# Kernel tuning notes

Measured on AMD Instinct MI355X. Metric: run time of the kernel, lower is better.

Reference implementation:

```python
import jax, jax.numpy as jnp
import numpy as np

N_CLASSES = 1000
FEAT_DIM = 256
N = 65536


def setup_inputs() -> dict:
    key = jax.random.key(0)
    k1, k2, k3 = jax.random.split(key, 3)
    gt = jax.random.randint(k1, (N, N_CLASSES), 0, 2, dtype=jnp.int32)
    features = jax.random.normal(k2, (N, FEAT_DIM), dtype=jnp.float32)
    centers = jax.random.normal(k3, (N_CLASSES, FEAT_DIM), dtype=jnp.float32)
    return {"gt": gt, "features": features, "centers": centers}


def reference(gt, features, centers):
    # loss = (1/N) * sum_c sum_{i : gt[i,c] > 0} ||features[i] - centers[c]||^2
    # Vectorized via ||f||^2 + ||c||^2 - 2 f.c  (replaces the per-class python loop)
    mask = (gt > 0).astype(features.dtype)                      # [N, C]
    f_sq = jnp.sum(features * features, axis=1)                 # [N]
    c_sq = jnp.sum(centers * centers, axis=1)                   # [C]
    cross = features @ centers.T                                # [N, C]
    dist = f_sq[:, None] + c_sq[None, :] - 2.0 * cross          # [N, C]
    num_instances = features.shape[0]
    return jnp.sum(mask * dist) / num_instances
```

## Files before the change

kernel.cpp:

```cpp
#include <hip/hip_runtime.h>
#include <stdint.h>

#define N_ROWS 65536
#define N_CLS  1000
#define KPAD   1024
#define FEAT   256
#define MT     64
#define NSTG   32
#define NIT    16

typedef short bf16x8 __attribute__((ext_vector_type(8)));
typedef float f32x4  __attribute__((ext_vector_type(4)));

__device__ __forceinline__ ushort f32_to_bf16_rne(float f) {
    union { float f; uint32_t u; } x; x.f = f;
    uint32_t u = x.u + 0x7FFFu + ((x.u >> 16) & 1u);
    return (ushort)(u >> 16);
}

__global__ __launch_bounds__(256) void prep_kernel(const float* __restrict__ centers,
                                                   ushort* __restrict__ Bfrag,
                                                   float* __restrict__ csq,
                                                   float* __restrict__ out) {
    const int c = blockIdx.x;
    const int n = threadIdx.x;
    float v = 0.f;
    if (c < N_CLS) v = centers[(size_t)c * FEAT + n];

    const int s    = c >> 5;
    const int quad = (c >> 3) & 3;
    const int j    = c & 7;
    const int w    = n >> 6;
    const int nt   = (n >> 4) & 3;
    const int ml   = n & 15;
    const int lane = quad * 16 + ml;
    const size_t idx = (((size_t)(s * 4 + w) * 4 + nt) * 64 + lane) * 8 + j;
    Bfrag[idx] = f32_to_bf16_rne(v);

    float sq = v * v;
    #pragma unroll
    for (int off = 32; off > 0; off >>= 1) sq += __shfl_down(sq, off);
    __shared__ float red[4];
    if ((threadIdx.x & 63) == 0) red[threadIdx.x >> 6] = sq;
    __syncthreads();
    if (threadIdx.x == 0) {
        csq[c] = red[0] + red[1] + red[2] + red[3];
        if (c == 0) out[0] = 0.f;
    }
}


__global__ __launch_bounds__(256) void compress_kernel(const int* __restrict__ gt,
                                                       const float* __restrict__ csq,
                                                       ushort* __restrict__ bitmask,
                                                       float* __restrict__ rowcnt,
                                                       float* __restrict__ t2row) {
    __shared__ float csqS[KPAD];
    const int tid  = threadIdx.x;
    *(float4*)&csqS[tid * 4] = *(const float4*)&csq[tid * 4];
    __syncthreads();
    const int lane = tid & 63;
    const int wid  = blockIdx.x * 4 + (tid >> 6);

    float4 cs[4];
    #pragma unroll
    for (int j = 0; j < 4; j++) cs[j] = *(const float4*)&csqS[j * 256 + lane * 4];
    const bool v3 = (768 + lane * 4) < N_CLS;

    auto ldrow = [&](int row, int4 (&d)[4]) {
        const int* g = gt + (size_t)row * N_CLS + lane * 4;
        d[0] = *(const int4*)(g);
        d[1] = *(const int4*)(g + 256);
        d[2] = *(const int4*)(g + 512);
        d[3] = v3 ? *(const int4*)(g + 768) : make_int4(0, 0, 0, 0);
    };
    auto proc = [&](int row, const int4 (&d)[4]) {
        uint32_t p =
              (uint32_t)d[0].x        | ((uint32_t)d[0].y << 1)  | ((uint32_t)d[0].z << 2)  | ((uint32_t)d[0].w << 3)
            | ((uint32_t)d[1].x << 4) | ((uint32_t)d[1].y << 5)  | ((uint32_t)d[1].z << 6)  | ((uint32_t)d[1].w << 7)
            | ((uint32_t)d[2].x << 8) | ((uint32_t)d[2].y << 9)  | ((uint32_t)d[2].z << 10) | ((uint32_t)d[2].w << 11)
            | ((uint32_t)d[3].x << 12)| ((uint32_t)d[3].y << 13) | ((uint32_t)d[3].z << 14) | ((uint32_t)d[3].w << 15);
        float t = (float)d[0].x * cs[0].x + (float)d[0].y * cs[0].y
                + (float)d[0].z * cs[0].z + (float)d[0].w * cs[0].w
                + (float)d[1].x * cs[1].x + (float)d[1].y * cs[1].y
                + (float)d[1].z * cs[1].z + (float)d[1].w * cs[1].w
                + (float)d[2].x * cs[2].x + (float)d[2].y * cs[2].y
                + (float)d[2].z * cs[2].z + (float)d[2].w * cs[2].w
                + (float)d[3].x * cs[3].x + (float)d[3].y * cs[3].y
                + (float)d[3].z * cs[3].z + (float)d[3].w * cs[3].w;
        int rc = __popc(p);
        #pragma unroll
        for (int off = 1; off < 64; off <<= 1) {
            rc += __shfl_xor(rc, off);
            t  += __shfl_xor(t, off);
        }
        bitmask[(size_t)row * 64 + lane] = (ushort)p;
        if (lane == 0) { rowcnt[row] = (float)rc; t2row[row] = t; }
    };

    int4 dP[4], dQ[4];
    ldrow(wid, dP);
    ldrow(wid + 8192, dQ);
    #pragma unroll
    for (int rr = 0; rr < 8; rr += 2) {
        if (rr + 2 < 8) { proc(wid + rr * 8192, dP); ldrow(wid + (rr + 2) * 8192, dP); }
        else              proc(wid + rr * 8192, dP);
        if (rr + 3 < 8) { proc(wid + (rr + 1) * 8192, dQ); ldrow(wid + (rr + 3) * 8192, dQ); }
        else              proc(wid + (rr + 1) * 8192, dQ);
    }
}

__global__ __launch_bounds__(256, 3) void main2_kernel(const ushort* __restrict__ bitmask,
                                                       const float* __restrict__ features,
                                                       const ushort* __restrict__ Bfrag,
                                                       const float* __restrict__ rowcnt,
                                                       const float* __restrict__ t2row,
                                                       float* __restrict__ out) {
    __shared__ uint32_t bmS[MT * 33];
    __shared__ float    rcS[MT], t2S[MT], blockred[4];

    const int tid  = threadIdx.x;
    const int lane = tid & 63;
    const int w    = tid >> 6;
    const int ml   = lane & 15;
    const int quad = lane >> 4;
    const int m0   = blockIdx.x * MT;

    const uint32_t* bm = (const uint32_t*)bitmask + (size_t)m0 * 32;
    #pragma unroll
    for (int i = 0; i < 8; i++) {
        int idx = i * 256 + tid;
        bmS[(idx >> 5) * 33 + (idx & 31)] = bm[idx];
    }
    if (tid < MT) rcS[tid] = rowcnt[m0 + tid];
    else if (tid < 2 * MT) t2S[tid - MT] = t2row[m0 + tid - MT];
    __syncthreads();

    f32x4 acc[4][4];
    #pragma unroll
    for (int i = 0; i < 4; i++)
        #pragma unroll
        for (int j = 0; j < 4; j++)
            #pragma unroll
            for (int k = 0; k < 4; k++) acc[i][j][k] = 0.f;

    const ushort* bb = Bfrag + ((size_t)w * 4 * 64 + lane) * 8;
    auto ld_B = [&](int s, bf16x8 (&b)[4]) {
        const ushort* p = bb + (size_t)s * 8192;
        b[0] = *(const bf16x8*)(p);
        b[1] = *(const bf16x8*)(p + 512);
        b[2] = *(const bf16x8*)(p + 1024);
        b[3] = *(const bf16x8*)(p + 1536);
    };

    auto dostage = [&](int s, const bf16x8 (&b)[4]) {
        const int dw = (s & 7) * 4 + quad;
        const int sb = (s >> 3) * 4;
        #pragma unroll
        for (int mt = 0; mt < 4; mt++) {
            const uint32_t W = bmS[(mt * 16 + ml) * 33 + dw];
            union { uint32_t u[4]; bf16x8 v; } a;
            #pragma unroll
            for (int p = 0; p < 4; p++) {
                const int b0 = (p < 2) ? (sb + 2 * p) : (16 + sb + 2 * (p - 2));
                a.u[p] = ((W >> b0) & 1u) * 0x3F80u
                       | ((W >> (b0 + 1)) & 1u) * 0x3F800000u;
            }
            #pragma unroll
            for (int nt = 0; nt < 4; nt++)
                acc[mt][nt] = __builtin_amdgcn_mfma_f32_16x16x32_bf16(
                    a.v, b[nt], acc[mt][nt], 0, 0, 0);
        }
    };

    bf16x8 BfP[4], BfQ[4];
    ld_B(0, BfP);
    ld_B(1, BfQ);
    for (int s = 0; s < NSTG; s += 2) {
        dostage(s, BfP);
        if (s + 2 < NSTG) ld_B(s + 2, BfP);
        dostage(s + 1, BfQ);
        if (s + 3 < NSTG) ld_B(s + 3, BfQ);
    }

    float part = 0.f;
    #pragma unroll
    for (int mt = 0; mt < 4; mt++) {
        #pragma unroll
        for (int nt = 0; nt < 4; nt++) {
            const int n = w * 64 + nt * 16 + ml;
            #pragma unroll
            for (int reg = 0; reg < 4; reg++) {
                const int ri = mt * 16 + quad * 4 + reg;
                const float f = features[(size_t)(m0 + ri) * FEAT + n];
                part += f * (rcS[ri] * f - 2.f * acc[mt][nt][reg]) + t2S[ri] * (1.f / 256.f);
            }
        }
    }
    #pragma unroll
    for (int off = 32; off > 0; off >>= 1) part += __shfl_down(part, off);
    if (lane == 0) blockred[w] = part;
    __syncthreads();
    if (tid == 0)
        atomicAdd(out, (blockred[0] + blockred[1] + blockred[2] + blockred[3]) *
                           (1.f / (float)N_ROWS));
}

__global__ __launch_bounds__(256, 3) void fused_kernel(const int* __restrict__ gt,
                                                       const float* __restrict__ features,
                                                       const ushort* __restrict__ Bfrag,
                                                       const float* __restrict__ csq,
                                                       float* __restrict__ out) {
    __shared__ ushort As[2 * 2 * 4 * 64 * 8];
    __shared__ float  csqS[KPAD];
    __shared__ float  rcS[256], t2S[256], rowcnt[MT], t2row[MT], blockred[4];

    const int tid  = threadIdx.x;
    const int m0   = blockIdx.x * MT;
    const int r    = tid >> 2;
    const int kc   = tid & 3;
    const int lane = tid & 63;
    const int w    = tid >> 6;
    const int ml   = lane & 15;
    const int quad = lane >> 4;

    f32x4 acc[4][4];
    #pragma unroll
    for (int i = 0; i < 4; i++)
        #pragma unroll
        for (int j = 0; j < 4; j++)
            #pragma unroll
            for (int k = 0; k < 4; k++) acc[i][j][k] = 0.f;

    int   rci = 0;
    float t2  = 0.f;
    const int* gtrow = gt + (size_t)(m0 + r) * N_CLS;

    const int mt_w = r >> 4, ml_w = r & 15;
    const int ks_w = kc >> 1, qb = (kc & 1) * 2;
    const int xw   = (ml_w >> 3) | (ks_w << 1) | ((kc & 1) << 2);
    const int slot0 = (((ks_w * 4 + mt_w) * 64) + (qb * 16 + ml_w)) ^ xw;
    const int slot1 = (((ks_w * 4 + mt_w) * 64) + ((qb + 1) * 16 + ml_w)) ^ xw;
    ushort* const wptr0 = As + slot0 * 8;
    ushort* const wptr1 = As + slot1 * 8;

    const int xr0 = ((lane >> 3) & 1) | (((lane >> 5) & 1) << 2);
    const int lx0 = (lane ^ xr0) * 8;
    const int lx1 = (lane ^ (xr0 | 2)) * 8;

    auto load_gt = [&](int it, int (&vv)[16]) {
        const int kb = it * 64 + kc * 16;
        if (kb + 16 <= N_CLS) {
            const int4* p = (const int4*)(gtrow + kb);
            int4 a0 = p[0], a1 = p[1], a2 = p[2], a3 = p[3];
            vv[0]=a0.x;  vv[1]=a0.y;  vv[2]=a0.z;  vv[3]=a0.w;
            vv[4]=a1.x;  vv[5]=a1.y;  vv[6]=a1.z;  vv[7]=a1.w;
            vv[8]=a2.x;  vv[9]=a2.y;  vv[10]=a2.z; vv[11]=a2.w;
            vv[12]=a3.x; vv[13]=a3.y; vv[14]=a3.z; vv[15]=a3.w;
        } else {
            #pragma unroll
            for (int j = 0; j < 16; j++) {
                int k = kb + j;
                vv[j] = (k < N_CLS) ? gtrow[k] : 0;
            }
        }
    };

    auto convert_store = [&](int buf, int it, const int (&vv)[16]) {
        const int kb = it * 64 + kc * 16;
        const float4* cp = (const float4*)&csqS[kb];
        float4 q0 = cp[0], q1 = cp[1], q2 = cp[2], q3 = cp[3];
        float cs[16] = {q0.x,q0.y,q0.z,q0.w, q1.x,q1.y,q1.z,q1.w,
                        q2.x,q2.y,q2.z,q2.w, q3.x,q3.y,q3.z,q3.w};
        uint32_t u[8];
        #pragma unroll
        for (int j = 0; j < 8; j++)
            u[j] = (uint32_t)(vv[2*j] + (vv[2*j+1] << 16)) * 0x3F80u;
        #pragma unroll
        for (int j = 0; j < 16; j++) { rci += vv[j]; t2 += (float)vv[j] * cs[j]; }
        uint4* d0 = (uint4*)(wptr0 + buf * 4096);
        uint4* d1 = (uint4*)(wptr1 + buf * 4096);
        *d0 = make_uint4(u[0], u[1], u[2], u[3]);
        *d1 = make_uint4(u[4], u[5], u[6], u[7]);
    };

    const ushort* bbase = Bfrag + ((size_t)w * 4) * 64 * 8 + (size_t)lane * 8;
    auto mfma_iter = [&](int buf, int it) {
        bf16x8 b0[4], b1[4];
        const ushort* p0 = bbase + (size_t)(it * 2 + 0) * (4 * 4 * 64 * 8);
        const ushort* p1 = bbase + (size_t)(it * 2 + 1) * (4 * 4 * 64 * 8);
        #pragma unroll
        for (int nt = 0; nt < 4; ++nt) b0[nt] = *(const bf16x8*)(p0 + nt * 64 * 8);
        #pragma unroll
        for (int nt = 0; nt < 4; ++nt) b1[nt] = *(const bf16x8*)(p1 + nt * 64 * 8);
        #pragma unroll
        for (int ks = 0; ks < 2; ++ks) {
            const int lx = ks ? lx1 : lx0;
            bf16x8 af[4];
            #pragma unroll
            for (int mt = 0; mt < 4; mt++)
                af[mt] = *(const bf16x8*)(As + buf * 4096 + (ks * 4 + mt) * 512 + lx);
            #pragma unroll
            for (int mt = 0; mt < 4; mt++)
                #pragma unroll
                for (int nt = 0; nt < 4; nt++)
                    acc[mt][nt] = __builtin_amdgcn_mfma_f32_16x16x32_bf16(
                        af[mt], ks ? b1[nt] : b0[nt], acc[mt][nt], 0, 0, 0);
        }
    };

    int gtA[16], gtB[16];
    {
        *(float4*)&csqS[tid * 4] = *(const float4*)&csq[tid * 4];
        load_gt(0, gtA);
        __syncthreads();
        convert_store(0, 0, gtA);
        load_gt(1, gtA);
        __syncthreads();
    }
    for (int it = 0; it < NIT; it += 2) {
        if (it + 2 < NIT) load_gt(it + 2, gtB);
        mfma_iter(0, it);
        if (it + 1 < NIT) convert_store(1, it + 1, gtA);
        __syncthreads();
        if (it + 3 < NIT) load_gt(it + 3, gtA);
        mfma_iter(1, it + 1);
        if (it + 2 < NIT) convert_store(0, it + 2, gtB);
        __syncthreads();
    }

    rcS[tid] = (float)rci;
    t2S[tid] = t2;
    __syncthreads();
    if (tid < MT) {
        rowcnt[tid] = rcS[tid*4] + rcS[tid*4+1] + rcS[tid*4+2] + rcS[tid*4+3];
        t2row[tid]  = t2S[tid*4] + t2S[tid*4+1] + t2S[tid*4+2] + t2S[tid*4+3];
    }
    __syncthreads();

    float part = 0.f;
    #pragma unroll
    for (int mt = 0; mt < 4; mt++) {
        #pragma unroll
        for (int nt = 0; nt < 4; nt++) {
            const int n = w * 64 + nt * 16 + ml;
            #pragma unroll
            for (int reg = 0; reg < 4; reg++) {
                const int ri = mt * 16 + quad * 4 + reg;
                const float f = features[(size_t)(m0 + ri) * FEAT + n];
                part += f * (rowcnt[ri] * f - 2.f * acc[mt][nt][reg]) + t2row[ri] * (1.f / 256.f);
            }
        }
    }
    #pragma unroll
    for (int off = 32; off > 0; off >>= 1) part += __shfl_down(part, off);
    if (lane == 0) blockred[w] = part;
    __syncthreads();
    if (tid == 0)
        atomicAdd(out, (blockred[0] + blockred[1] + blockred[2] + blockred[3]) *
                           (1.f / (float)N_ROWS));
}

extern "C" void kernel_launch(void* const* d_in, const int* in_sizes, int n_in,
                              void* d_out, int out_size, void* d_ws, size_t ws_size,
                              hipStream_t stream) {
    const int*   gt       = (const int*)d_in[0];
    const float* features = (const float*)d_in[1];
    const float* centers  = (const float*)d_in[2];
    float*       out      = (float*)d_out;

    char* ws = (char*)d_ws;
    ushort* Bfrag = (ushort*)(ws);
    float*  csq   = (float*)(ws + 524288);

    prep_kernel<<<KPAD, 256, 0, stream>>>(centers, Bfrag, csq, out);

    const size_t REQ = 524288u + 4096u + 262144u + 262144u + 8388608u;
    if (ws_size >= REQ) {
        float*  rowcnt  = (float*)(ws + 528384);
        float*  t2row   = (float*)(ws + 790528);
        ushort* bitmask = (ushort*)(ws + 1052672);
        compress_kernel<<<2048, 256, 0, stream>>>(gt, csq, bitmask, rowcnt, t2row);
        main2_kernel<<<N_ROWS / MT, 256, 0, stream>>>(bitmask, features, Bfrag,
                                                      rowcnt, t2row, out);
    } else {
        fused_kernel<<<N_ROWS / MT, 256, 0, stream>>>(gt, features, Bfrag, csq, out);
    }
}
```

Before: 432.7 us.

## Move per-row count and center-norm sums from compress into main kernel

The compress kernel now only packs gt into bitmasks, dropping its per-row popcount, masked csq dot product, wave reductions and the rowcnt/t2row writes. Each row's mask count and sum of masked center norms are now computed in main2 from the shared-memory bitmask and a permuted csq table (csqB) built by prep. Compress also processes eight consecutive rows per wave instead of rows strided across the grid. This shortens the memory-bound compress pass and removes two intermediate arrays, but adds bit-test work and an extra 4 KB of shared memory to each main2 block, which could reduce occupancy or lengthen its prologue.

```diff
diff --git a/kernel.cpp b/kernel.cpp
--- a/kernel.cpp
+++ b/kernel.cpp
@@ -21,6 +21,7 @@
 __global__ __launch_bounds__(256) void prep_kernel(const float* __restrict__ centers,
                                                    ushort* __restrict__ Bfrag,
                                                    float* __restrict__ csq,
+                                                   float* __restrict__ csqB,
                                                    float* __restrict__ out) {
     const int c = blockIdx.x;
     const int n = threadIdx.x;
@@ -44,28 +45,23 @@
     if ((threadIdx.x & 63) == 0) red[threadIdx.x >> 6] = sq;
     __syncthreads();
     if (threadIdx.x == 0) {
-        csq[c] = red[0] + red[1] + red[2] + red[3];
+        const float total = red[0] + red[1] + red[2] + red[3];
+        csq[c] = total;
+        const int l   = (c & 255) >> 2;
+        const int j2  = c >> 8;
+        const int i2  = c & 3;
+        csqB[(l >> 1) * 32 + (l & 1) * 16 + j2 * 4 + i2] = total;
         if (c == 0) out[0] = 0.f;
     }
 }
 
 
 __global__ __launch_bounds__(256) void compress_kernel(const int* __restrict__ gt,
-                                                       const float* __restrict__ csq,
-                                                       ushort* __restrict__ bitmask,
-                                                       float* __restrict__ rowcnt,
-                                                       float* __restrict__ t2row) {
-    __shared__ float csqS[KPAD];
-    const int tid  = threadIdx.x;
-    *(float4*)&csqS[tid * 4] = *(const float4*)&csq[tid * 4];
-    __syncthreads();
-    const int lane = tid & 63;
-    const int wid  = blockIdx.x * 4 + (tid >> 6);
-
-    float4 cs[4];
-    #pragma unroll
-    for (int j = 0; j < 4; j++) cs[j] = *(const float4*)&csqS[j * 256 + lane * 4];
-    const bool v3 = (768 + lane * 4) < N_CLS;
+                                                       ushort* __restrict__ bitmask) {
+    const int lane = threadIdx.x & 63;
+    const int wid  = blockIdx.x * 4 + (threadIdx.x >> 6);
+    const int base = wid * 8;
+    const bool v3  = (768 + lane * 4) < N_CLS;
 
     auto ldrow = [&](int row, int4 (&d)[4]) {
         const int* g = gt + (size_t)row * N_CLS + lane * 4;
@@ -74,49 +70,36 @@
         d[2] = *(const int4*)(g + 512);
         d[3] = v3 ? *(const int4*)(g + 768) : make_int4(0, 0, 0, 0);
     };
-    auto proc = [&](int row, const int4 (&d)[4]) {
-        uint32_t p =
-              (uint32_t)d[0].x        | ((uint32_t)d[0].y << 1)  | ((uint32_t)d[0].z << 2)  | ((uint32_t)d[0].w << 3)
-            | ((uint32_t)d[1].x << 4) | ((uint32_t)d[1].y << 5)  | ((uint32_t)d[1].z << 6)  | ((uint32_t)d[1].w << 7)
-            | ((uint32_t)d[2].x << 8) | ((uint32_t)d[2].y << 9)  | ((uint32_t)d[2].z << 10) | ((uint32_t)d[2].w << 11)
-            | ((uint32_t)d[3].x << 12)| ((uint32_t)d[3].y << 13) | ((uint32_t)d[3].z << 14) | ((uint32_t)d[3].w << 15);
-        float t = (float)d[0].x * cs[0].x + (float)d[0].y * cs[0].y
-                + (float)d[0].z * cs[0].z + (float)d[0].w * cs[0].w
-                + (float)d[1].x * cs[1].x + (float)d[1].y * cs[1].y
-                + (float)d[1].z * cs[1].z + (float)d[1].w * cs[1].w
-                + (float)d[2].x * cs[2].x + (float)d[2].y * cs[2].y
-                + (float)d[2].z * cs[2].z + (float)d[2].w * cs[2].w
-                + (float)d[3].x * cs[3].x + (float)d[3].y * cs[3].y
-                + (float)d[3].z * cs[3].z + (float)d[3].w * cs[3].w;
-        int rc = __popc(p);
-        #pragma unroll
-        for (int off = 1; off < 64; off <<= 1) {
-            rc += __shfl_xor(rc, off);
-            t  += __shfl_xor(t, off);
-        }
-        bitmask[(size_t)row * 64 + lane] = (ushort)p;
-        if (lane == 0) { rowcnt[row] = (float)rc; t2row[row] = t; }
+    auto pack = [&](const int4 (&d)[4]) -> uint32_t {
+        return (uint32_t)d[0].x        | ((uint32_t)d[0].y << 1)  | ((uint32_t)d[0].z << 2)  | ((uint32_t)d[0].w << 3)
+            | ((uint32_t)d[1].x << 4)  | ((uint32_t)d[1].y << 5)  | ((uint32_t)d[1].z << 6)  | ((uint32_t)d[1].w << 7)
+            | ((uint32_t)d[2].x << 8)  | ((uint32_t)d[2].y << 9)  | ((uint32_t)d[2].z << 10) | ((uint32_t)d[2].w << 11)
+            | ((uint32_t)d[3].x << 12) | ((uint32_t)d[3].y << 13) | ((uint32_t)d[3].z << 14) | ((uint32_t)d[3].w << 15);
     };
 
     int4 dP[4], dQ[4];
-    ldrow(wid, dP);
-    ldrow(wid + 8192, dQ);
+    ldrow(base, dP);
+    ldrow(base + 1, dQ);
     #pragma unroll
     for (int rr = 0; rr < 8; rr += 2) {
-        if (rr + 2 < 8) { proc(wid + rr * 8192, dP); ldrow(wid + (rr + 2) * 8192, dP); }
-        else              proc(wid + rr * 8192, dP);
-        if (rr + 3 < 8) { proc(wid + (rr + 1) * 8192, dQ); ldrow(wid + (rr + 3) * 8192, dQ); }
-        else              proc(wid + (rr + 1) * 8192, dQ);
+        uint32_t p0 = pack(dP);
+        if (rr + 2 < 8) ldrow(base + rr + 2, dP);
+        bitmask[(size_t)(base + rr) * 64 + lane] = (ushort)p0;
+        uint32_t p1 = pack(dQ);
+        if (rr + 3 < 8) ldrow(base + rr + 3, dQ);
+        bitmask[(size_t)(base + rr + 1) * 64 + lane] = (ushort)p1;
     }
 }
 
 __global__ __launch_bounds__(256, 3) void main2_kernel(const ushort* __restrict__ bitmask,
                                                        const float* __restrict__ features,
                                                        const ushort* __restrict__ Bfrag,
-                                                       const float* __restrict__ rowcnt,
-                                                       const float* __restrict__ t2row,
+                                                       const float* __restrict__ csqB,
                                                        float* __restrict__ out) {
     __shared__ uint32_t bmS[MT * 33];
+    __shared__ float    csqBS[KPAD];
+    __shared__ float    rcP[4][MT];
+    __shared__ float    t2P[4][MT];
     __shared__ float    rcS[MT], t2S[MT], blockred[4];
 
     const int tid  = threadIdx.x;
@@ -132,8 +115,35 @@
         int idx = i * 256 + tid;
         bmS[(idx >> 5) * 33 + (idx & 31)] = bm[idx];
     }
-    if (tid < MT) rcS[tid] = rowcnt[m0 + tid];
-    else if (tid < 2 * MT) t2S[tid - MT] = t2row[m0 + tid - MT];
+    *(float4*)&csqBS[tid * 4] = *(const float4*)&csqB[tid * 4];
+    __syncthreads();
+
+    {
+        const int ri = tid & 63;
+        float rc = 0.f, t = 0.f;
+        #pragma unroll
+        for (int jj = 0; jj < 8; jj++) {
+            const int dw = w * 8 + jj;
+            const uint32_t W = bmS[ri * 33 + dw];
+            rc += (float)__popc(W);
+            const float4* cb = (const float4*)&csqBS[dw * 32];
+            #pragma unroll
+            for (int q4 = 0; q4 < 8; q4++) {
+                float4 c4 = cb[q4];
+                t += ((W >> (q4 * 4 + 0)) & 1u) ? c4.x : 0.f;
+                t += ((W >> (q4 * 4 + 1)) & 1u) ? c4.y : 0.f;
+                t += ((W >> (q4 * 4 + 2)) & 1u) ? c4.z : 0.f;
+                t += ((W >> (q4 * 4 + 3)) & 1u) ? c4.w : 0.f;
+            }
+        }
+        rcP[w][ri] = rc;
+        t2P[w][ri] = t;
+    }
+    __syncthreads();
+    if (tid < MT) {
+        rcS[tid] = rcP[0][tid] + rcP[1][tid] + rcP[2][tid] + rcP[3][tid];
+        t2S[tid] = t2P[0][tid] + t2P[1][tid] + t2P[2][tid] + t2P[3][tid];
+    }
     __syncthreads();
 
     f32x4 acc[4][4];
@@ -372,17 +382,16 @@
     char* ws = (char*)d_ws;
     ushort* Bfrag = (ushort*)(ws);
     float*  csq   = (float*)(ws + 524288);
-
-    prep_kernel<<<KPAD, 256, 0, stream>>>(centers, Bfrag, csq, out);
-
-    const size_t REQ = 524288u + 4096u + 262144u + 262144u + 8388608u;
+    float*  csqB  = (float*)(ws + 528384);
+
+    prep_kernel<<<KPAD, 256, 0, stream>>>(centers, Bfrag, csq, csqB, out);
+
+    const size_t REQ = 532480u + 8388608u;
     if (ws_size >= REQ) {
-        float*  rowcnt  = (float*)(ws + 528384);
-        float*  t2row   = (float*)(ws + 790528);
-        ushort* bitmask = (ushort*)(ws + 1052672);
-        compress_kernel<<<2048, 256, 0, stream>>>(gt, csq, bitmask, rowcnt, t2row);
+        ushort* bitmask = (ushort*)(ws + 532480);
+        compress_kernel<<<2048, 256, 0, stream>>>(gt, bitmask);
         main2_kernel<<<N_ROWS / MT, 256, 0, stream>>>(bitmask, features, Bfrag,
-                                                      rowcnt, t2row, out);
+                                                      csqB, out);
     } else {
         fused_kernel<<<N_ROWS / MT, 256, 0, stream>>>(gt, features, Bfrag, csq, out);
     }
```

Result: slower. 444.1 us (+2.6%).
